# Kernel tuning notes

Measured on AMD Instinct MI355X. Metric: run time of the kernel, lower is better.

The kernel has to match this reference:

```python
import jax, jax.numpy as jnp
import numpy as np

N, E = 50000, 800000
IN, HID, OUT, EH = 128, 64, 128, 32  # node dims, edge-MLP hidden=32
N_ETYPES, N_NTYPES = 3, 2


def setup_inputs() -> dict:
    key = jax.random.key(0)
    ks = jax.random.split(key, 12)
    w = lambda k, shape, fan: jax.random.normal(k, shape, jnp.float32) / np.float32(np.sqrt(fan))
    nf = jax.random.normal(ks[0], (N, IN), jnp.float32)
    edge_index = jax.random.randint(ks[1], (2, E), 0, N, dtype=jnp.int32)
    edge_type = jax.random.randint(ks[2], (E,), 0, N_ETYPES, dtype=jnp.int32)
    node_type = jax.random.randint(ks[3], (N,), 0, N_NTYPES, dtype=jnp.int32)
    return {
        "nf": nf,
        "edge_index": edge_index,
        "edge_type": edge_type,
        "node_type": node_type,
        # layer 0: 128 -> 64
        "eW0": w(ks[4], (N_ETYPES, 2 * IN, EH), 2 * IN),
        "eb0": jax.random.normal(ks[5], (N_ETYPES, EH), jnp.float32) * 0.01,
        "nW0": w(ks[6], (N_NTYPES, N_ETYPES * EH, HID), N_ETYPES * EH),
        "nb0": jax.random.normal(ks[7], (N_NTYPES, HID), jnp.float32) * 0.01,
        # layer 1: 64 -> 128
        "eW1": w(ks[8], (N_ETYPES, 2 * HID, EH), 2 * HID),
        "eb1": jax.random.normal(ks[9], (N_ETYPES, EH), jnp.float32) * 0.01,
        "nW1": w(ks[10], (N_NTYPES, N_ETYPES * EH, OUT), N_ETYPES * EH),
        "nb1": jax.random.normal(ks[11], (N_NTYPES, OUT), jnp.float32) * 0.01,
    }


def _layer(nf, eW, eb, nW, nb, src, dst, edge_type, node_type):
    """One GraphNeuralNetLayer: per-edge-type message MLP + mean-scatter, then per-node-type update MLP."""
    n = nf.shape[0]
    # edge gather + concat: [E, 2*in]
    feat = jnp.concatenate([nf[src], nf[dst]], axis=-1)
    msgs = []
    for e in range(eW.shape[0]):  # fixed, small number of edge types
        m = jax.nn.relu(feat @ eW[e] + eb[e])            # [E, EH]
        mask = (edge_type == e).astype(nf.dtype)          # select this edge type
        s = jax.ops.segment_sum(m * mask[:, None], dst, num_segments=n)
        cnt = jax.ops.segment_sum(mask, dst, num_segments=n)
        # mean over mailbox; nodes with no type-e in-edges get zeros
        msgs.append(s / jnp.maximum(cnt, 1.0)[:, None])
    h = jnp.concatenate(msgs, axis=-1)                    # [N, 3*EH]
    out0 = jax.nn.relu(h @ nW[0] + nb[0])
    out1 = jax.nn.relu(h @ nW[1] + nb[1])
    return jnp.where((node_type == 0)[:, None], out0, out1)


def reference(nf, edge_index, edge_type, node_type, eW0, eb0, nW0, nb0, eW1, eb1, nW1, nb1):
    src, dst = edge_index[0], edge_index[1]
    h = _layer(nf, eW0, eb0, nW0, nb0, src, dst, edge_type, node_type)   # [N, 64]
    return _layer(h, eW1, eb1, nW1, nb1, src, dst, edge_type, node_type) # [N, 128]
```

## Files before the change

kernel.cpp:

```cpp
#include <hip/hip_runtime.h>


typedef __attribute__((ext_vector_type(8))) short bf16x8_t;
typedef __attribute__((ext_vector_type(4))) float f32x4_t;

__device__ __forceinline__ void cvt_split(float x, unsigned short& h, unsigned short& l) {
  unsigned u = __float_as_uint(x);
  unsigned rh = u + 0x7FFFu + ((u >> 16) & 1u);
  h = (unsigned short)(rh >> 16);
  float xh = __uint_as_float((unsigned)h << 16);
  float xl = x - xh;
  unsigned v = __float_as_uint(xl);
  unsigned rl = v + 0x7FFFu + ((v >> 16) & 1u);
  l = (unsigned short)(rl >> 16);
}


__global__ __launch_bounds__(256) void rank_kernel(const int* __restrict__ dst,
                                                   int* __restrict__ deg8,
                                                   int* __restrict__ rank, int E) {
  int i = blockIdx.x * 256 + threadIdx.x;
  if (i < E) {
    int d = dst[i];
    int r = (i >> 8) & 7;
    rank[i] = atomicAdd(&deg8[d * 8 + r], 1);
  }
}

__global__ __launch_bounds__(256) void scan1_kernel(int* __restrict__ deg8,
                                                    int* __restrict__ rowstart,
                                                    int* __restrict__ bsum, int n) {
  __shared__ int tmp[256];
  int t = threadIdx.x;
  int base = blockIdx.x * 1024 + t * 4;
  int vdeg[4];
#pragma unroll
  for (int q = 0; q < 4; ++q) {
    int v = base + q;
    int d = 0;
    if (v < n) {
      int4 a = *(int4*)(deg8 + (size_t)v * 8);
      int4 b = *(int4*)(deg8 + (size_t)v * 8 + 4);
      int p1 = a.x, p2 = p1 + a.y, p3 = p2 + a.z, p4 = p3 + a.w;
      int p5 = p4 + b.x, p6 = p5 + b.y, p7 = p6 + b.z;
      d = p7 + b.w;
      *(int4*)(deg8 + (size_t)v * 8) = make_int4(0, p1, p2, p3);
      *(int4*)(deg8 + (size_t)v * 8 + 4) = make_int4(p4, p5, p6, p7);
    }
    vdeg[q] = d;
  }
  int s = vdeg[0] + vdeg[1] + vdeg[2] + vdeg[3];
  tmp[t] = s;
  __syncthreads();
  for (int off = 1; off < 256; off <<= 1) {
    int u = (t >= off) ? tmp[t - off] : 0;
    __syncthreads();
    tmp[t] += u;
    __syncthreads();
  }
  int excl = tmp[t] - s;
  if (base < n)     rowstart[base]     = excl;
  if (base + 1 < n) rowstart[base + 1] = excl + vdeg[0];
  if (base + 2 < n) rowstart[base + 2] = excl + vdeg[0] + vdeg[1];
  if (base + 3 < n) rowstart[base + 3] = excl + vdeg[0] + vdeg[1] + vdeg[2];
  if (t == 255) bsum[blockIdx.x] = tmp[255];
}

__global__ __launch_bounds__(64) void scan2_kernel(const int* __restrict__ bsum,
                                                   int* __restrict__ boff, int nb,
                                                   int* __restrict__ rowstart, int n) {
  int lane = threadIdx.x;
  int v = (lane < nb) ? bsum[lane] : 0;
  int incl = v;
  for (int off = 1; off < 64; off <<= 1) {
    int u = __shfl_up(incl, off, 64);
    if (lane >= off) incl += u;
  }
  if (lane < nb) boff[lane] = incl - v;
  if (lane == 63) rowstart[n] = incl;
}

__global__ __launch_bounds__(256) void scan3_kernel(int* __restrict__ rowstart,
                                                    const int* __restrict__ boff, int n) {
  int i = blockIdx.x * 256 + threadIdx.x;
  if (i < n) rowstart[i] += boff[i >> 10];
}

__global__ __launch_bounds__(256) void fill_kernel(const int* __restrict__ src,
                                                   const int* __restrict__ dst,
                                                   const int* __restrict__ etype,
                                                   const int* __restrict__ rank,
                                                   const int* __restrict__ rowstart,
                                                   const int* __restrict__ deg8,
                                                   int* __restrict__ edata, int E) {
  int i = blockIdx.x * 256 + threadIdx.x;
  if (i < E) {
    int d = dst[i];
    int r = (i >> 8) & 7;
    int et = etype[i];
    int pos = rowstart[d] + deg8[d * 8 + r] + rank[i];
    edata[pos] = src[i] * 768 + et * 129;
  }
}


__global__ __launch_bounds__(256) void partition_kernel(const int* __restrict__ ntype,
                                                        int* __restrict__ idxbuf,
                                                        int* __restrict__ tcnt,
                                                        int n, int ncap) {
  int i = blockIdx.x * 256 + threadIdx.x;
  int lane = threadIdx.x & 63;
  int t = (i < n) ? ntype[i] : -1;
  unsigned long long m0 = __ballot(t == 0);
  unsigned long long m1 = __ballot(t == 1);
  int b0 = 0, b1 = 0;
  if (lane == 0) {
    b0 = atomicAdd(&tcnt[0], (int)__popcll(m0));
    b1 = atomicAdd(&tcnt[1], (int)__popcll(m1));
  }
  b0 = __shfl(b0, 0);
  b1 = __shfl(b1, 0);
  unsigned long long below = (1ull << lane) - 1ull;
  if (t == 0) idxbuf[b0 + (int)__popcll(m0 & below)] = i;
  else if (t == 1) idxbuf[ncap + b1 + (int)__popcll(m1 & below)] = i;
}


template <int IN>
__global__ __launch_bounds__(256) void prep_w(const float* __restrict__ eW,
                                              float* __restrict__ wfh,
                                              float* __restrict__ wfl) {
  constexpr int KC = IN / 32;
  int id = blockIdx.x * 256 + threadIdx.x;
  if (id >= 12 * KC * 64) return;
  int lane = id & 63;
  int fk = id >> 6;
  int kc = fk % KC, ct = fk / KC;
  int n = ct * 16 + (lane & 15);
  int kb = kc * 32 + ((lane >> 4) & 3) * 8;
  int half = (n >= 96) ? 1 : 0;
  int jj = n - 96 * half;
  int e = jj >> 5, o = jj & 31;
  const float* wp = eW + ((size_t)((e * 2 + half) * IN) + kb) * 32 + o;
  bf16x8_t hv, lv;
#pragma unroll
  for (int j = 0; j < 8; ++j) {
    unsigned short h, l;
    cvt_split(wp[(size_t)j * 32], h, l);
    hv[j] = (short)h;
    lv[j] = (short)l;
  }
  *(bf16x8_t*)(wfh + (size_t)id * 4) = hv;
  *(bf16x8_t*)(wfl + (size_t)id * 4) = lv;
}


template <int IN>
__global__ __launch_bounds__(256) void proj_mfma(const float* __restrict__ X,
                                                 const float* __restrict__ wfh,
                                                 const float* __restrict__ wfl,
                                                 float* __restrict__ P, int n) {
  constexpr int KC = IN / 32;
  __shared__ short Ah[4 * KC * 64 * 8];
  __shared__ short Al[4 * KC * 64 * 8];
  const int tx = threadIdx.x;
  const int base = blockIdx.x * 64;

  for (int q = tx; q < 4 * KC * 64; q += 256) {
    int lane = q & 63;
    int fk = q >> 6;
    int kc = fk % KC, nt = fk / KC;
    int node = base + nt * 16 + (lane & 15);
    int kb = kc * 32 + ((lane >> 4) & 3) * 8;
    float xs[8];
    if (node < n) {
      float4 a = *(const float4*)(X + (size_t)node * IN + kb);
      float4 b = *(const float4*)(X + (size_t)node * IN + kb + 4);
      xs[0] = a.x; xs[1] = a.y; xs[2] = a.z; xs[3] = a.w;
      xs[4] = b.x; xs[5] = b.y; xs[6] = b.z; xs[7] = b.w;
    } else {
#pragma unroll
      for (int j = 0; j < 8; ++j) xs[j] = 0.f;
    }
    bf16x8_t hv, lv;
#pragma unroll
    for (int j = 0; j < 8; ++j) {
      unsigned short h, l;
      cvt_split(xs[j], h, l);
      hv[j] = (short)h;
      lv[j] = (short)l;
    }
    *(bf16x8_t*)(Ah + (size_t)q * 8) = hv;
    *(bf16x8_t*)(Al + (size_t)q * 8) = lv;
  }
  __syncthreads();

  const int wave = tx >> 6;
  const int lane = tx & 63;

  f32x4_t acc[4][3];
#pragma unroll
  for (int nt = 0; nt < 4; ++nt)
#pragma unroll
    for (int c = 0; c < 3; ++c) acc[nt][c] = (f32x4_t){0.f, 0.f, 0.f, 0.f};

  for (int kc = 0; kc < KC; ++kc) {
    bf16x8_t Bh[3], Bl[3];
#pragma unroll
    for (int c = 0; c < 3; ++c) {
      int ct = wave * 3 + c;
      size_t idx = ((size_t)(ct * KC + kc) * 64 + lane) * 4;
      Bh[c] = *(const bf16x8_t*)(wfh + idx);
      Bl[c] = *(const bf16x8_t*)(wfl + idx);
    }
#pragma unroll
    for (int nt = 0; nt < 4; ++nt) {
      size_t idx = ((size_t)(nt * KC + kc) * 64 + lane) * 8;
      bf16x8_t ah = *(const bf16x8_t*)(Ah + idx);
      bf16x8_t al = *(const bf16x8_t*)(Al + idx);
#pragma unroll
      for (int c = 0; c < 3; ++c) {
        acc[nt][c] = __builtin_amdgcn_mfma_f32_16x16x32_bf16(ah, Bh[c], acc[nt][c], 0, 0, 0);
        acc[nt][c] = __builtin_amdgcn_mfma_f32_16x16x32_bf16(ah, Bl[c], acc[nt][c], 0, 0, 0);
        acc[nt][c] = __builtin_amdgcn_mfma_f32_16x16x32_bf16(al, Bh[c], acc[nt][c], 0, 0, 0);
      }
    }
  }

  const int row0 = ((lane >> 4) & 3) * 4;
  const int col = lane & 15;
#pragma unroll
  for (int nt = 0; nt < 4; ++nt) {
#pragma unroll
    for (int c = 0; c < 3; ++c) {
      int jcol = (wave * 3 + c) * 16 + col;
#pragma unroll
      for (int r = 0; r < 4; ++r) {
        int node = base + nt * 16 + row0 + r;
        if (node < n) P[(size_t)node * 192 + jcol] = acc[nt][c][r];
      }
    }
  }
}


#define ACC_EDGE(pk, v)                                      \
  {                                                          \
    int et_ = (pk) & 3;                                      \
    float pb_ = (et_ == 0) ? pdb0 : ((et_ == 1) ? pdb1 : pdb2); \
    float m_ = fmaxf((v) + pb_, 0.f);                        \
    a0 += (et_ == 0) ? m_ : 0.f;                             \
    a1 += (et_ == 1) ? m_ : 0.f;                             \
    a2 += (et_ == 2) ? m_ : 0.f;                             \
    c0 += (et_ == 0);                                        \
    c1 += (et_ == 1);                                        \
  }

__global__ __launch_bounds__(256) void aggregate_kernel(const float* __restrict__ P,
                                                        const int* __restrict__ rowstart,
                                                        const int* __restrict__ edata,
                                                        const float* __restrict__ eb,
                                                        float* __restrict__ h, int n) {
  int wid = (blockIdx.x * 256 + threadIdx.x) >> 6;
  if (wid >= n) return;
  int lane = threadIdx.x & 63;
  int o = lane & 31, slot = lane >> 5;
  const float* Pd = P + (size_t)wid * 192 + 96;
  float pdb0 = Pd[o] + eb[o];
  float pdb1 = Pd[32 + o] + eb[32 + o];
  float pdb2 = Pd[64 + o] + eb[64 + o];
  int s = rowstart[wid], e = rowstart[wid + 1];
  const char* Pb = (const char*)P;
  int o4 = o * 4;
  float a0 = 0.f, a1 = 0.f, a2 = 0.f;
  int c0 = 0, c1 = 0;
  int i = s + slot;
  for (; i + 6 < e; i += 8) {
    int p0 = edata[i];
    int p1 = edata[i + 2];
    int p2 = edata[i + 4];
    int p3 = edata[i + 6];
    float v0 = *(const float*)(Pb + (p0 & ~3) + o4);
    float v1 = *(const float*)(Pb + (p1 & ~3) + o4);
    float v2 = *(const float*)(Pb + (p2 & ~3) + o4);
    float v3 = *(const float*)(Pb + (p3 & ~3) + o4);
    ACC_EDGE(p0, v0)
    ACC_EDGE(p1, v1)
    ACC_EDGE(p2, v2)
    ACC_EDGE(p3, v3)
  }
  for (; i < e; i += 2) {
    int pk = edata[i];
    float v = *(const float*)(Pb + (pk & ~3) + o4);
    ACC_EDGE(pk, v)
  }
  a0 += __shfl_xor(a0, 32);
  a1 += __shfl_xor(a1, 32);
  a2 += __shfl_xor(a2, 32);
  c0 += __shfl_xor(c0, 32);
  c1 += __shfl_xor(c1, 32);
  if (slot == 0) {
    int total = e - s;
    float* hn = h + (size_t)wid * 96;
    hn[o] = a0 / fmaxf((float)c0, 1.f);
    hn[32 + o] = a1 / fmaxf((float)c1, 1.f);
    hn[64 + o] = a2 / fmaxf((float)(total - c0 - c1), 1.f);
  }
}


template <int OUT>
__global__ __launch_bounds__(256) void mlp2_kernel(const float* __restrict__ H,
                                                   const float* __restrict__ nW,
                                                   const float* __restrict__ nb,
                                                   const int* __restrict__ idxbuf,
                                                   const int* __restrict__ tcnt,
                                                   float* __restrict__ out, int ncap) {
  constexpr int CO = OUT / 32;
  __shared__ float Xs[64 * 32];
  __shared__ float Ws[8 * OUT * 4];

  int c0 = tcnt[0];
  int nb0 = (c0 + 63) >> 6;
  int t, base, cnt;
  if ((int)blockIdx.x < nb0) {
    t = 0; base = blockIdx.x << 6; cnt = c0;
  } else {
    t = 1; base = ((int)blockIdx.x - nb0) << 6; cnt = tcnt[1];
    if (base >= cnt) return;
  }
  const float* W = nW + (size_t)t * 96 * OUT;
  const float* bias = nb + t * OUT;
  const int* il = idxbuf + (size_t)t * ncap;

  const int tx = threadIdx.x;
  const int t32 = tx & 31;
  const int ng = tx >> 5;

  float acc[8][CO];
#pragma unroll
  for (int i = 0; i < 8; ++i)
#pragma unroll
    for (int c = 0; c < CO; ++c) acc[i][c] = 0.f;

  for (int k0 = 0; k0 < 96; k0 += 32) {
    for (int id = tx; id < 512; id += 256) {
      int i = id >> 3, kk4 = (id & 7) * 4;
      float4 v = make_float4(0.f, 0.f, 0.f, 0.f);
      if (base + i < cnt) {
        int row = il[base + i];
        v = *(const float4*)(H + (size_t)row * 96 + k0 + kk4);
      }
      *(float4*)(Xs + i * 32 + kk4) = v;
    }
    for (int id = tx; id < 8 * OUT; id += 256) {
      int g = id / OUT;
      int j = id % OUT;
      const float* wp = W + (size_t)(k0 + 4 * g) * OUT + j;
      float4 v = make_float4(wp[0], wp[OUT], wp[2 * OUT], wp[3 * OUT]);
      *(float4*)(Ws + (size_t)id * 4) = v;
    }
    __syncthreads();
#pragma unroll
    for (int g = 0; g < 8; ++g) {
      float4 xv[8], wv[CO];
#pragma unroll
      for (int i = 0; i < 8; ++i) xv[i] = *(const float4*)(Xs + (ng * 8 + i) * 32 + 4 * g);
#pragma unroll
      for (int c = 0; c < CO; ++c) wv[c] = *(const float4*)(Ws + ((size_t)g * OUT + t32 + 32 * c) * 4);
#pragma unroll
      for (int i = 0; i < 8; ++i)
#pragma unroll
        for (int c = 0; c < CO; ++c) {
          acc[i][c] = fmaf(xv[i].x, wv[c].x, acc[i][c]);
          acc[i][c] = fmaf(xv[i].y, wv[c].y, acc[i][c]);
          acc[i][c] = fmaf(xv[i].z, wv[c].z, acc[i][c]);
          acc[i][c] = fmaf(xv[i].w, wv[c].w, acc[i][c]);
        }
    }
    __syncthreads();
  }

  float bj[CO];
#pragma unroll
  for (int c = 0; c < CO; ++c) bj[c] = bias[t32 + 32 * c];
#pragma unroll
  for (int i = 0; i < 8; ++i) {
    int slot = base + ng * 8 + i;
    if (slot < cnt) {
      int row = il[slot];
#pragma unroll
      for (int c = 0; c < CO; ++c)
        out[(size_t)row * OUT + t32 + 32 * c] = fmaxf(acc[i][c] + bj[c], 0.f);
    }
  }
}


extern "C" void kernel_launch(void* const* d_in, const int* in_sizes, int n_in,
                              void* d_out, int out_size, void* d_ws, size_t ws_size,
                              hipStream_t stream) {
  const float* nf    = (const float*)d_in[0];
  const int*   eidx  = (const int*)d_in[1];
  const int*   etype = (const int*)d_in[2];
  const int*   ntype = (const int*)d_in[3];
  const float* eW0   = (const float*)d_in[4];
  const float* eb0   = (const float*)d_in[5];
  const float* nW0   = (const float*)d_in[6];
  const float* nb0   = (const float*)d_in[7];
  const float* eW1   = (const float*)d_in[8];
  const float* eb1   = (const float*)d_in[9];
  const float* nW1   = (const float*)d_in[10];
  const float* nb1   = (const float*)d_in[11];
  const int N = in_sizes[3];
  const int E = in_sizes[2];
  const int* srcv = eidx;
  const int* dstv = eidx + E;

  float* P   = (float*)d_ws;
  float* h96 = P + (size_t)N * 192;
  float* h64 = h96 + (size_t)N * 96;
  int* rowstart = (int*)(h64 + (size_t)N * 64);
  int* tcnt     = rowstart + ((N + 4) & ~3);
  int* bsum     = tcnt + 2;
  int* boff     = bsum + 64;
  int* idxbuf   = boff + 64;
  int* edata    = idxbuf + 2 * N;
  float* wf0h   = (float*)(edata + E);
  float* wf0l   = wf0h + 12288;
  float* wf1h   = wf0l + 12288;
  float* wf1l   = wf1h + 6144;
  int* rank     = (int*)h96;
  int* deg8     = (int*)h64;

  const int nsb = (N + 1023) / 1024;
  const int egrid = (E + 255) / 256;

  hipMemsetAsync(deg8, 0, (size_t)N * 8 * sizeof(int), stream);
  hipMemsetAsync(tcnt, 0, 2 * sizeof(int), stream);
  prep_w<128><<<12, 256, 0, stream>>>(eW0, wf0h, wf0l);
  prep_w<64><<<6, 256, 0, stream>>>(eW1, wf1h, wf1l);
  rank_kernel<<<egrid, 256, 0, stream>>>(dstv, deg8, rank, E);
  scan1_kernel<<<nsb, 256, 0, stream>>>(deg8, rowstart, bsum, N);
  scan2_kernel<<<1, 64, 0, stream>>>(bsum, boff, nsb, rowstart, N);
  scan3_kernel<<<(N + 255) / 256, 256, 0, stream>>>(rowstart, boff, N);
  fill_kernel<<<egrid, 256, 0, stream>>>(srcv, dstv, etype, rank, rowstart, deg8, edata, E);
  partition_kernel<<<(N + 255) / 256, 256, 0, stream>>>(ntype, idxbuf, tcnt, N, N);

  const int pgrid = (N + 63) / 64;
  int agrid = (N + 3) / 4;
  int mgrid = (N + 63) / 64 + 2;

  proj_mfma<128><<<pgrid, 256, 0, stream>>>(nf, wf0h, wf0l, P, N);
  aggregate_kernel<<<agrid, 256, 0, stream>>>(P, rowstart, edata, eb0, h96, N);
  mlp2_kernel<64><<<mgrid, 256, 0, stream>>>(h96, nW0, nb0, idxbuf, tcnt, h64, N);

  proj_mfma<64><<<pgrid, 256, 0, stream>>>(h64, wf1h, wf1l, P, N);
  aggregate_kernel<<<agrid, 256, 0, stream>>>(P, rowstart, edata, eb1, h96, N);
  mlp2_kernel<128><<<mgrid, 256, 0, stream>>>(h96, nW1, nb1, idxbuf, tcnt, (float*)d_out, N);
}
```

Before: 316.4 us.

## Vectorize edge aggregation with float4 gathers and fold scan3 and memsets into kernels

The aggregate kernel now gives each lane a float4 slice of the 32-wide message. Eight edges are processed in parallel per wave instead of two, with 128-byte row gathers and a wider shuffle reduction at the end. The scan3 pass is removed: the block offset is added on the fly where rowstart is read, in the fill and aggregate kernels. The two memsets are folded into prep_w and scan2, which cuts several launches from the preprocessing chain. The cost is an extra boff load per access and more accumulator registers in the aggregate kernel.

```diff
diff --git a/kernel.cpp b/kernel.cpp
--- a/kernel.cpp
+++ b/kernel.cpp
@@ -68,8 +68,10 @@
 
 __global__ __launch_bounds__(64) void scan2_kernel(const int* __restrict__ bsum,
                                                    int* __restrict__ boff, int nb,
-                                                   int* __restrict__ rowstart, int n) {
+                                                   int* __restrict__ rowstart, int n,
+                                                   int* __restrict__ tcnt) {
   int lane = threadIdx.x;
+  if (lane < 2) tcnt[lane] = 0;
   int v = (lane < nb) ? bsum[lane] : 0;
   int incl = v;
   for (int off = 1; off < 64; off <<= 1) {
@@ -80,17 +82,12 @@
   if (lane == 63) rowstart[n] = incl;
 }
 
-__global__ __launch_bounds__(256) void scan3_kernel(int* __restrict__ rowstart,
-                                                    const int* __restrict__ boff, int n) {
-  int i = blockIdx.x * 256 + threadIdx.x;
-  if (i < n) rowstart[i] += boff[i >> 10];
-}
-
 __global__ __launch_bounds__(256) void fill_kernel(const int* __restrict__ src,
                                                    const int* __restrict__ dst,
                                                    const int* __restrict__ etype,
                                                    const int* __restrict__ rank,
                                                    const int* __restrict__ rowstart,
+                                                   const int* __restrict__ boff,
                                                    const int* __restrict__ deg8,
                                                    int* __restrict__ edata, int E) {
   int i = blockIdx.x * 256 + threadIdx.x;
@@ -98,7 +95,7 @@
     int d = dst[i];
     int r = (i >> 8) & 7;
     int et = etype[i];
-    int pos = rowstart[d] + deg8[d * 8 + r] + rank[i];
+    int pos = rowstart[d] + boff[d >> 10] + deg8[d * 8 + r] + rank[i];
     edata[pos] = src[i] * 768 + et * 129;
   }
 }
@@ -129,9 +126,15 @@
 template <int IN>
 __global__ __launch_bounds__(256) void prep_w(const float* __restrict__ eW,
                                               float* __restrict__ wfh,
-                                              float* __restrict__ wfl) {
+                                              float* __restrict__ wfl,
+                                              int* __restrict__ zbuf, int zn4) {
   constexpr int KC = IN / 32;
   int id = blockIdx.x * 256 + threadIdx.x;
+  if (zbuf) {
+    int4* zb = (int4*)zbuf;
+    int tot = gridDim.x * 256;
+    for (int z = id; z < zn4; z += tot) zb[z] = make_int4(0, 0, 0, 0);
+  }
   if (id >= 12 * KC * 64) return;
   int lane = id & 63;
   int fk = id >> 6;
@@ -244,67 +247,88 @@
 }
 
 
-#define ACC_EDGE(pk, v)                                      \
-  {                                                          \
-    int et_ = (pk) & 3;                                      \
-    float pb_ = (et_ == 0) ? pdb0 : ((et_ == 1) ? pdb1 : pdb2); \
-    float m_ = fmaxf((v) + pb_, 0.f);                        \
-    a0 += (et_ == 0) ? m_ : 0.f;                             \
-    a1 += (et_ == 1) ? m_ : 0.f;                             \
-    a2 += (et_ == 2) ? m_ : 0.f;                             \
-    c0 += (et_ == 0);                                        \
-    c1 += (et_ == 1);                                        \
+#define ACC_EDGE4(pk, v)                                              \
+  {                                                                   \
+    int et_ = (pk) & 3;                                               \
+    float4 pb_ = (et_ == 0) ? pdb0 : ((et_ == 1) ? pdb1 : pdb2);      \
+    float mx_ = fmaxf((v).x + pb_.x, 0.f);                            \
+    float my_ = fmaxf((v).y + pb_.y, 0.f);                            \
+    float mz_ = fmaxf((v).z + pb_.z, 0.f);                            \
+    float mw_ = fmaxf((v).w + pb_.w, 0.f);                            \
+    bool e0_ = (et_ == 0), e1_ = (et_ == 1), e2_ = (et_ == 2);        \
+    a0.x += e0_ ? mx_ : 0.f; a0.y += e0_ ? my_ : 0.f;                 \
+    a0.z += e0_ ? mz_ : 0.f; a0.w += e0_ ? mw_ : 0.f;                 \
+    a1.x += e1_ ? mx_ : 0.f; a1.y += e1_ ? my_ : 0.f;                 \
+    a1.z += e1_ ? mz_ : 0.f; a1.w += e1_ ? mw_ : 0.f;                 \
+    a2.x += e2_ ? mx_ : 0.f; a2.y += e2_ ? my_ : 0.f;                 \
+    a2.z += e2_ ? mz_ : 0.f; a2.w += e2_ ? mw_ : 0.f;                 \
+    c0 += e0_; c1 += e1_;                                             \
   }
 
 __global__ __launch_bounds__(256) void aggregate_kernel(const float* __restrict__ P,
                                                         const int* __restrict__ rowstart,
+                                                        const int* __restrict__ boff,
                                                         const int* __restrict__ edata,
                                                         const float* __restrict__ eb,
                                                         float* __restrict__ h, int n) {
   int wid = (blockIdx.x * 256 + threadIdx.x) >> 6;
   if (wid >= n) return;
   int lane = threadIdx.x & 63;
-  int o = lane & 31, slot = lane >> 5;
+  int co = (lane & 7) * 4;
+  int cb = co * 4;
+  int slot = lane >> 3;
   const float* Pd = P + (size_t)wid * 192 + 96;
-  float pdb0 = Pd[o] + eb[o];
-  float pdb1 = Pd[32 + o] + eb[32 + o];
-  float pdb2 = Pd[64 + o] + eb[64 + o];
-  int s = rowstart[wid], e = rowstart[wid + 1];
+  float4 pdb0 = *(const float4*)(Pd + co);
+  float4 pdb1 = *(const float4*)(Pd + 32 + co);
+  float4 pdb2 = *(const float4*)(Pd + 64 + co);
+  float4 ebv;
+  ebv = *(const float4*)(eb + co);
+  pdb0.x += ebv.x; pdb0.y += ebv.y; pdb0.z += ebv.z; pdb0.w += ebv.w;
+  ebv = *(const float4*)(eb + 32 + co);
+  pdb1.x += ebv.x; pdb1.y += ebv.y; pdb1.z += ebv.z; pdb1.w += ebv.w;
+  ebv = *(const float4*)(eb + 64 + co);
+  pdb2.x += ebv.x; pdb2.y += ebv.y; pdb2.z += ebv.z; pdb2.w += ebv.w;
+
+  int s = rowstart[wid] + boff[wid >> 10];
+  int e = rowstart[wid + 1] + ((wid + 1 < n) ? boff[(wid + 1) >> 10] : 0);
   const char* Pb = (const char*)P;
-  int o4 = o * 4;
-  float a0 = 0.f, a1 = 0.f, a2 = 0.f;
+  float4 a0 = make_float4(0.f, 0.f, 0.f, 0.f);
+  float4 a1 = a0, a2 = a0;
   int c0 = 0, c1 = 0;
   int i = s + slot;
-  for (; i + 6 < e; i += 8) {
+  for (; i + 8 < e; i += 16) {
     int p0 = edata[i];
-    int p1 = edata[i + 2];
-    int p2 = edata[i + 4];
-    int p3 = edata[i + 6];
-    float v0 = *(const float*)(Pb + (p0 & ~3) + o4);
-    float v1 = *(const float*)(Pb + (p1 & ~3) + o4);
-    float v2 = *(const float*)(Pb + (p2 & ~3) + o4);
-    float v3 = *(const float*)(Pb + (p3 & ~3) + o4);
-    ACC_EDGE(p0, v0)
-    ACC_EDGE(p1, v1)
-    ACC_EDGE(p2, v2)
-    ACC_EDGE(p3, v3)
-  }
-  for (; i < e; i += 2) {
+    int p1 = edata[i + 8];
+    float4 v0 = *(const float4*)(Pb + (size_t)(p0 & ~3) + cb);
+    float4 v1 = *(const float4*)(Pb + (size_t)(p1 & ~3) + cb);
+    ACC_EDGE4(p0, v0)
+    ACC_EDGE4(p1, v1)
+  }
+  for (; i < e; i += 8) {
     int pk = edata[i];
-    float v = *(const float*)(Pb + (pk & ~3) + o4);
-    ACC_EDGE(pk, v)
-  }
-  a0 += __shfl_xor(a0, 32);
-  a1 += __shfl_xor(a1, 32);
-  a2 += __shfl_xor(a2, 32);
-  c0 += __shfl_xor(c0, 32);
-  c1 += __shfl_xor(c1, 32);
+    float4 v = *(const float4*)(Pb + (size_t)(pk & ~3) + cb);
+    ACC_EDGE4(pk, v)
+  }
+#pragma unroll
+  for (int off = 8; off < 64; off <<= 1) {
+    a0.x += __shfl_xor(a0.x, off); a0.y += __shfl_xor(a0.y, off);
+    a0.z += __shfl_xor(a0.z, off); a0.w += __shfl_xor(a0.w, off);
+    a1.x += __shfl_xor(a1.x, off); a1.y += __shfl_xor(a1.y, off);
+    a1.z += __shfl_xor(a1.z, off); a1.w += __shfl_xor(a1.w, off);
+    a2.x += __shfl_xor(a2.x, off); a2.y += __shfl_xor(a2.y, off);
+    a2.z += __shfl_xor(a2.z, off); a2.w += __shfl_xor(a2.w, off);
+    c0 += __shfl_xor(c0, off);
+    c1 += __shfl_xor(c1, off);
+  }
   if (slot == 0) {
     int total = e - s;
+    float d0 = fmaxf((float)c0, 1.f);
+    float d1 = fmaxf((float)c1, 1.f);
+    float d2 = fmaxf((float)(total - c0 - c1), 1.f);
     float* hn = h + (size_t)wid * 96;
-    hn[o] = a0 / fmaxf((float)c0, 1.f);
-    hn[32 + o] = a1 / fmaxf((float)c1, 1.f);
-    hn[64 + o] = a2 / fmaxf((float)(total - c0 - c1), 1.f);
+    *(float4*)(hn + co)      = make_float4(a0.x / d0, a0.y / d0, a0.z / d0, a0.w / d0);
+    *(float4*)(hn + 32 + co) = make_float4(a1.x / d1, a1.y / d1, a1.z / d1, a1.w / d1);
+    *(float4*)(hn + 64 + co) = make_float4(a2.x / d2, a2.y / d2, a2.z / d2, a2.w / d2);
   }
 }
 
@@ -436,26 +460,23 @@
   const int nsb = (N + 1023) / 1024;
   const int egrid = (E + 255) / 256;
 
-  hipMemsetAsync(deg8, 0, (size_t)N * 8 * sizeof(int), stream);
-  hipMemsetAsync(tcnt, 0, 2 * sizeof(int), stream);
-  prep_w<128><<<12, 256, 0, stream>>>(eW0, wf0h, wf0l);
-  prep_w<64><<<6, 256, 0, stream>>>(eW1, wf1h, wf1l);
+  prep_w<128><<<12, 256, 0, stream>>>(eW0, wf0h, wf0l, deg8, N * 2);
+  prep_w<64><<<6, 256, 0, stream>>>(eW1, wf1h, wf1l, nullptr, 0);
   rank_kernel<<<egrid, 256, 0, stream>>>(dstv, deg8, rank, E);
   scan1_kernel<<<nsb, 256, 0, stream>>>(deg8, rowstart, bsum, N);
-  scan2_kernel<<<1, 64, 0, stream>>>(bsum, boff, nsb, rowstart, N);
-  scan3_kernel<<<(N + 255) / 256, 256, 0, stream>>>(rowstart, boff, N);
-  fill_kernel<<<egrid, 256, 0, stream>>>(srcv, dstv, etype, rank, rowstart, deg8, edata, E);
+  scan2_kernel<<<1, 64, 0, stream>>>(bsum, boff, nsb, rowstart, N, tcnt);
   partition_kernel<<<(N + 255) / 256, 256, 0, stream>>>(ntype, idxbuf, tcnt, N, N);
+  fill_kernel<<<egrid, 256, 0, stream>>>(srcv, dstv, etype, rank, rowstart, boff, deg8, edata, E);
 
   const int pgrid = (N + 63) / 64;
   int agrid = (N + 3) / 4;
   int mgrid = (N + 63) / 64 + 2;
 
   proj_mfma<128><<<pgrid, 256, 0, stream>>>(nf, wf0h, wf0l, P, N);
-  aggregate_kernel<<<agrid, 256, 0, stream>>>(P, rowstart, edata, eb0, h96, N);
+  aggregate_kernel<<<agrid, 256, 0, stream>>>(P, rowstart, boff, edata, eb0, h96, N);
   mlp2_kernel<64><<<mgrid, 256, 0, stream>>>(h96, nW0, nb0, idxbuf, tcnt, h64, N);
 
   proj_mfma<64><<<pgrid, 256, 0, stream>>>(h64, wf1h, wf1l, P, N);
-  aggregate_kernel<<<agrid, 256, 0, stream>>>(P, rowstart, edata, eb1, h96, N);
+  aggregate_kernel<<<agrid, 256, 0, stream>>>(P, rowstart, boff, edata, eb1, h96, N);
   mlp2_kernel<128><<<mgrid, 256, 0, stream>>>(h96, nW1, nb1, idxbuf, tcnt, (float*)d_out, N);
 }
```

Result: slower. 330.9 us (+4.6%).
